# Optimization experiments

Measured on AMD Instinct MI355X. Metric: run time of the kernel, lower is better.

## Reference

```python
import jax, jax.numpy as jnp
import numpy as np
from jax import lax

DN = ('NCHW', 'OIHW', 'NCHW')
BN_EPS = 1e-5


def _conv(x, w, pad):
    # pad: list of (lo, hi) for H, W
    return lax.conv_general_dilated(x, w, (1, 1), pad, dimension_numbers=DN)


def _grid_sample_bilinear(img, grid):
    """F.grid_sample(img, grid, align_corners=True, padding_mode='zeros').
    img: [N,C,H,W], grid: [N,Ho,Wo,2] with (x,y) in [-1,1]."""
    N, C, H, W = img.shape
    gx, gy = grid[..., 0], grid[..., 1]
    # align_corners=True mapping to pixel coords
    ix = (gx + 1.0) * 0.5 * (W - 1)
    iy = (gy + 1.0) * 0.5 * (H - 1)
    x0 = jnp.floor(ix)
    y0 = jnp.floor(iy)
    x1 = x0 + 1.0
    y1 = y0 + 1.0
    # bilinear weights
    wa = (x1 - ix) * (y1 - iy)  # top-left (x0,y0)
    wb = (ix - x0) * (y1 - iy)  # top-right (x1,y0)
    wc = (x1 - ix) * (iy - y0)  # bottom-left (x0,y1)
    wd = (ix - x0) * (iy - y0)  # bottom-right (x1,y1)

    imgc = jnp.transpose(img, (0, 2, 3, 1))  # [N,H,W,C]
    b = jnp.arange(N)[:, None, None]

    def gather(xi, yi):
        valid = (xi >= 0) & (xi <= W - 1) & (yi >= 0) & (yi <= H - 1)
        xc = jnp.clip(xi, 0, W - 1).astype(jnp.int32)
        yc = jnp.clip(yi, 0, H - 1).astype(jnp.int32)
        v = imgc[b, yc, xc]  # [N,Ho,Wo,C]
        return v * valid[..., None].astype(img.dtype)

    out = (gather(x0, y0) * wa[..., None] + gather(x1, y0) * wb[..., None]
           + gather(x0, y1) * wc[..., None] + gather(x1, y1) * wd[..., None])
    return jnp.transpose(out, (0, 3, 1, 2))  # [N,C,Ho,Wo]


def setup_inputs() -> dict:
    key = jax.random.key(0)
    ks = jax.random.split(key, 12)
    N, C1, C2 = 8, 512, 256
    H, W = 64, 64
    x1 = jax.random.normal(ks[0], (N, C1, 2 * H, 2 * W), dtype=jnp.float32)
    x2 = jax.random.normal(ks[1], (N, C2, H, W), dtype=jnp.float32)
    w_change = jax.random.normal(ks[2], (C2, C1, 1, 1), dtype=jnp.float32) * 0.02
    b_change = jax.random.normal(ks[3], (C2,), dtype=jnp.float32) * 0.02
    w_cc1 = jax.random.normal(ks[4], (C2, 2 * C2, 1, 1), dtype=jnp.float32) * 0.02
    bn_gamma = 1.0 + 0.1 * jax.random.normal(ks[5], (C2,), dtype=jnp.float32)
    bn_beta = 0.1 * jax.random.normal(ks[6], (C2,), dtype=jnp.float32)
    bn_mean = 0.1 * jax.random.normal(ks[7], (C2,), dtype=jnp.float32)
    bn_var = jax.random.uniform(ks[8], (C2,), dtype=jnp.float32, minval=0.5, maxval=1.5)
    w_cc2 = jax.random.normal(ks[9], (4, C2, 3, 3), dtype=jnp.float32) * 0.02
    return {"x1": x1, "x2": x2, "w_change": w_change, "b_change": b_change,
            "w_cc1": w_cc1, "bn_gamma": bn_gamma, "bn_beta": bn_beta,
            "bn_mean": bn_mean, "bn_var": bn_var, "w_cc2": w_cc2}


def reference(x1, x2, w_change, b_change, w_cc1, bn_gamma, bn_beta, bn_mean, bn_var, w_cc2):
    # MaxPool2d(2,2)
    x1p = lax.reduce_window(x1, -jnp.inf, lax.max, (1, 1, 2, 2), (1, 1, 2, 2), 'VALID')
    # change: 1x1 conv with bias
    x1c = _conv(x1p, w_change, [(0, 0), (0, 0)]) + b_change[None, :, None, None]
    # concat + concat_conv (1x1 conv -> BN(eval) -> ReLU -> 3x3 conv)
    x = jnp.concatenate([x1c, x2], axis=1)
    x = _conv(x, w_cc1, [(0, 0), (0, 0)])
    inv = lax.rsqrt(bn_var + BN_EPS)
    x = (x - bn_mean[None, :, None, None]) * (inv * bn_gamma)[None, :, None, None] + bn_beta[None, :, None, None]
    x = jax.nn.relu(x)
    flow = _conv(x, w_cc2, [(1, 1), (1, 1)])  # [N,4,H,W]
    flow1 = flow[:, :2]
    flow2 = flow[:, 2:]

    N, _, H, W = x1c.shape
    # base grid: [...,0]=x over width, [...,1]=y over height
    xs = jnp.linspace(-1.0, 1.0, W, dtype=x1c.dtype)
    ys = jnp.linspace(-1.0, 1.0, H, dtype=x1c.dtype)
    base = jnp.stack(jnp.meshgrid(xs, ys, indexing='xy'), axis=-1)  # [H,W,2]
    norm = jnp.array([(W - 1) / 2.0, (H - 1) / 2.0], dtype=x1c.dtype)

    grid1 = base[None] + jnp.transpose(flow1, (0, 2, 3, 1)) / norm
    grid2 = base[None] + jnp.transpose(flow2, (0, 2, 3, 1)) / norm

    u1 = _grid_sample_bilinear(x1c, grid1)
    u2 = _grid_sample_bilinear(x2, grid2)
    return u1 + u2
```

## Files before the change

kernel.cpp:

```cpp
#include <hip/hip_runtime.h>
#include <hip/hip_bf16.h>

#define NB 8
#define C1 512
#define C2 256
#define HWSZ 4096
#define BN_EPS 1e-5f
#define P2 264

typedef __hip_bfloat16 bf16;
typedef __hip_bfloat162 bf162;
typedef __attribute__((ext_vector_type(8))) short short8v;
typedef __attribute__((ext_vector_type(4))) float f32x4;

static __device__ inline float b2f(bf16 h) { return __bfloat162float(h); }

static __device__ inline unsigned short f2bf(float f) {
  union { bf16 h; unsigned short u; } c;
  c.h = __float2bfloat16(f);
  return c.u;
}

static __device__ inline unsigned pack2(float a, float b) {
  union { unsigned u; bf162 h; } pk;
  pk.h = __float22bfloat162_rn(make_float2(a, b));
  return pk.u;
}

static __device__ inline uint2 pack4(float a, float b, float c, float d) {
  union { uint2 u; bf162 h[2]; } pk;
  pk.h[0] = __float22bfloat162_rn(make_float2(a, b));
  pk.h[1] = __float22bfloat162_rn(make_float2(c, d));
  return pk.u;
}

#define SBARQ() asm volatile("s_waitcnt lgkmcnt(0)\n\ts_barrier" ::: "memory")
#define SBAR()  asm volatile("s_barrier" ::: "memory")
#define LGKM0() asm volatile("s_waitcnt lgkmcnt(0)" ::: "memory")

__global__ __launch_bounds__(256) void k0_swizzle(
    const float* __restrict__ wch, const float* __restrict__ wcc1,
    unsigned short* __restrict__ wchB, unsigned short* __restrict__ wcc1B) {
  const int t = blockIdx.x * 256 + threadIdx.x;
  const int which = t >> 17;
  const int r = t & 131071;
  const int i = r & 7;
  const int lane = (r >> 3) & 63;
  const int ntile = (r >> 9) & 15;
  const int kstep = r >> 13;
  const int ci = kstep * 32 + (lane >> 4) * 8 + i;
  const int co = ntile * 16 + (lane & 15);
  const float* s = which ? wcc1 : wch;
  unsigned short* d = which ? wcc1B : wchB;
  d[r] = f2bf(s[co * 512 + ci]);
}

__global__ __launch_bounds__(512) void k12_fused(
    const float* __restrict__ x1, const float* __restrict__ x2,
    const unsigned short* __restrict__ wchB, const unsigned short* __restrict__ wcc1B,
    const float* __restrict__ bch,
    const float* __restrict__ gamma, const float* __restrict__ beta,
    const float* __restrict__ mean, const float* __restrict__ var,
    bf16* __restrict__ x1c, bf16* __restrict__ xbn) {
  __shared__ unsigned short As[64 * 40];
  __shared__ unsigned short As2[64 * P2];
  const int tid = threadIdx.x;
  const int lane = tid & 63;
  const int wv = tid >> 6;
  const int lrow = lane & 15;
  const int lgrp = lane >> 4;

  const int m0g = blockIdx.x * 64;
  const int n = m0g >> 12;
  const int hw0 = m0g & 4095;
  const int h = hw0 >> 6;

  f32x4 acc[4][2];
#pragma unroll
  for (int mt = 0; mt < 4; ++mt)
#pragma unroll
    for (int nt = 0; nt < 2; ++nt) acc[mt][nt] = (f32x4){0.f, 0.f, 0.f, 0.f};

  const int pmi = tid & 31;
  const int ms = pmi * 2;
  const int ch0 = (tid >> 5) * 2;

  const float* x1p = x1 + (size_t)n * C1 * 16384 + (size_t)(2 * h) * 128 + 2 * ms;

  float4 t0, b0, t1, b1;
#define LOADA(K0_) do { \
    const float* p_ = x1p + (size_t)((K0_) + ch0) * 16384; \
    t0 = *(const float4*)p_;            b0 = *(const float4*)(p_ + 128); \
    t1 = *(const float4*)(p_ + 16384);  b1 = *(const float4*)(p_ + 16384 + 128); \
  } while (0)
#define POOLA(U0_, U1_) do { \
    U0_ = pack2(fmaxf(fmaxf(t0.x, t0.y), fmaxf(b0.x, b0.y)), \
                fmaxf(fmaxf(t1.x, t1.y), fmaxf(b1.x, b1.y))); \
    U1_ = pack2(fmaxf(fmaxf(t0.z, t0.w), fmaxf(b0.z, b0.w)), \
                fmaxf(fmaxf(t1.z, t1.w), fmaxf(b1.z, b1.w))); \
  } while (0)

  unsigned uA0, uA1;
  LOADA(0);
  POOLA(uA0, uA1);
  LOADA(32);

  for (int ks = 0; ks < 16; ++ks) {
    SBARQ();
    *(unsigned*)&As[ms * 40 + ch0] = uA0;
    *(unsigned*)&As[(ms + 1) * 40 + ch0] = uA1;
    LGKM0();
    SBAR();

    unsigned uN0, uN1;
    if (ks < 15) {
      POOLA(uN0, uN1);
      if (ks < 14) LOADA((ks + 2) * 32);
    }

    short8v a[4];
#pragma unroll
    for (int mt = 0; mt < 4; ++mt)
      a[mt] = *(const short8v*)&As[(mt * 16 + lrow) * 40 + lgrp * 8];
#pragma unroll
    for (int nt = 0; nt < 2; ++nt) {
      const int ntile = wv * 2 + nt;
      const short8v b = *(const short8v*)&wchB[(size_t)((ks * 16 + ntile) * 64 + lane) * 8];
#pragma unroll
      for (int mt = 0; mt < 4; ++mt)
        acc[mt][nt] = __builtin_amdgcn_mfma_f32_16x16x32_bf16(a[mt], b, acc[mt][nt], 0, 0, 0);
    }
    if (ks < 15) { uA0 = uN0; uA1 = uN1; }
  }

  const int chB = tid >> 4;
  const int mqB = (tid & 15) * 4;
  float4 cf0 = *(const float4*)&x2[((size_t)(n * C2 + chB)) * HWSZ + hw0 + mqB];
  float4 cf1 = *(const float4*)&x2[((size_t)(n * C2 + 32 + chB)) * HWSZ + hw0 + mqB];

#pragma unroll
  for (int nt = 0; nt < 2; ++nt) {
    const int co = (wv * 2 + nt) * 16 + lrow;
    const float bias = bch[co];
#pragma unroll
    for (int mt = 0; mt < 4; ++mt) {
      const f32x4 v = acc[mt][nt];
      const uint2 pk = pack4(v.x + bias, v.y + bias, v.z + bias, v.w + bias);
      *(uint2*)&x1c[((size_t)(n * C2 + co)) * HWSZ + hw0 + mt * 16 + lgrp * 4] = pk;
      const int mb = mt * 16 + lgrp * 4;
      As2[(mb + 0) * P2 + co] = (unsigned short)(pk.x & 0xffffu);
      As2[(mb + 1) * P2 + co] = (unsigned short)(pk.x >> 16);
      As2[(mb + 2) * P2 + co] = (unsigned short)(pk.y & 0xffffu);
      As2[(mb + 3) * P2 + co] = (unsigned short)(pk.y >> 16);
      acc[mt][nt] = (f32x4){0.f, 0.f, 0.f, 0.f};
    }
  }
  LGKM0();
  SBAR();

#pragma unroll
  for (int ks = 0; ks < 8; ++ks) {
    short8v a[4];
#pragma unroll
    for (int mt = 0; mt < 4; ++mt)
      a[mt] = *(const short8v*)&As2[(mt * 16 + lrow) * P2 + ks * 32 + lgrp * 8];
#pragma unroll
    for (int nt = 0; nt < 2; ++nt) {
      const int ntile = wv * 2 + nt;
      const short8v b = *(const short8v*)&wcc1B[(size_t)((ks * 16 + ntile) * 64 + lane) * 8];
#pragma unroll
      for (int mt = 0; mt < 4; ++mt)
        acc[mt][nt] = __builtin_amdgcn_mfma_f32_16x16x32_bf16(a[mt], b, acc[mt][nt], 0, 0, 0);
    }
  }

  for (int ks = 8; ks < 16; ++ks) {
    const unsigned p0 = pack2(cf0.x, cf0.y);
    const unsigned p1 = pack2(cf0.z, cf0.w);
    cf0 = cf1;
    if (ks < 14) {
      cf1 = *(const float4*)&x2[((size_t)(n * C2 + (ks - 6) * 32 + chB)) * HWSZ + hw0 + mqB];
    }
    SBARQ();
    As[(mqB + 0) * 40 + chB] = (unsigned short)(p0 & 0xffffu);
    As[(mqB + 1) * 40 + chB] = (unsigned short)(p0 >> 16);
    As[(mqB + 2) * 40 + chB] = (unsigned short)(p1 & 0xffffu);
    As[(mqB + 3) * 40 + chB] = (unsigned short)(p1 >> 16);
    LGKM0();
    SBAR();

    short8v a[4];
#pragma unroll
    for (int mt = 0; mt < 4; ++mt)
      a[mt] = *(const short8v*)&As[(mt * 16 + lrow) * 40 + lgrp * 8];
#pragma unroll
    for (int nt = 0; nt < 2; ++nt) {
      const int ntile = wv * 2 + nt;
      const short8v b = *(const short8v*)&wcc1B[(size_t)((ks * 16 + ntile) * 64 + lane) * 8];
#pragma unroll
      for (int mt = 0; mt < 4; ++mt)
        acc[mt][nt] = __builtin_amdgcn_mfma_f32_16x16x32_bf16(a[mt], b, acc[mt][nt], 0, 0, 0);
    }
  }

#pragma unroll
  for (int nt = 0; nt < 2; ++nt) {
    const int co = (wv * 2 + nt) * 16 + lrow;
    const float sc = gamma[co] * rsqrtf(var[co] + BN_EPS);
    const float sh = beta[co] - mean[co] * sc;
#pragma unroll
    for (int mt = 0; mt < 4; ++mt) {
      const f32x4 vv = acc[mt][nt];
      *(uint2*)&xbn[((size_t)(n * C2 + co)) * HWSZ + hw0 + mt * 16 + lgrp * 4] =
          pack4(fmaxf(vv.x * sc + sh, 0.f), fmaxf(vv.y * sc + sh, 0.f),
                fmaxf(vv.z * sc + sh, 0.f), fmaxf(vv.w * sc + sh, 0.f));
    }
  }
#undef LOADA
#undef POOLA
}

__global__ __launch_bounds__(1024) void k34_conv_sample(
    const bf16* __restrict__ xbn, const float* __restrict__ wcc2,
    const bf16* __restrict__ x1c, const float* __restrict__ x2,
    float* __restrict__ out) {
  __shared__ float wsm[9216];
  __shared__ float part[16][4][64];
  __shared__ float flr[4][64];
  const int tid = threadIdx.x;
  const int n = blockIdx.x >> 6;
  const int h = blockIdx.x & 63;
  const int wl = tid & 63;
  const int q = tid >> 6;

  for (int idx = tid; idx < 9216; idx += 1024) {
    const int f = idx / 2304;
    const int r = idx % 2304;
    const int ci = r / 9;
    const int t = r % 9;
    wsm[ci * 36 + (t / 3) * 12 + (t % 3) * 4 + f] = wcc2[idx];
  }
  __syncthreads();

  float acc[4] = {0.f, 0.f, 0.f, 0.f};
  {
    const bf16* base = xbn + ((size_t)(n * C2 + q * 16)) * HWSZ;
    const float* wq = wsm + (q * 16) * 36;
    for (int cc = 0; cc < 16; ++cc) {
      const bf16* src = base + (size_t)cc * HWSZ;
      const float* wc = wq + cc * 36;
#pragma unroll
      for (int dy = 0; dy < 3; ++dy) {
        const int y = h + dy - 1;
        if ((unsigned)y >= 64u) continue;
        const float v = b2f(src[y * 64 + wl]);
        float vm = __shfl_up(v, 1);
        float vp = __shfl_down(v, 1);
        if (wl == 0) vm = 0.f;
        if (wl == 63) vp = 0.f;
        const float4 wa = *(const float4*)&wc[dy * 12 + 0];
        const float4 wb = *(const float4*)&wc[dy * 12 + 4];
        const float4 wd = *(const float4*)&wc[dy * 12 + 8];
        acc[0] = fmaf(vm, wa.x, fmaf(v, wb.x, fmaf(vp, wd.x, acc[0])));
        acc[1] = fmaf(vm, wa.y, fmaf(v, wb.y, fmaf(vp, wd.y, acc[1])));
        acc[2] = fmaf(vm, wa.z, fmaf(v, wb.z, fmaf(vp, wd.z, acc[2])));
        acc[3] = fmaf(vm, wa.w, fmaf(v, wb.w, fmaf(vp, wd.w, acc[3])));
      }
    }
  }
  part[q][0][wl] = acc[0];
  part[q][1][wl] = acc[1];
  part[q][2][wl] = acc[2];
  part[q][3][wl] = acc[3];
  __syncthreads();
  if (tid < 256) {
    const int f = tid >> 6;
    const int ww = tid & 63;
    float s = 0.f;
#pragma unroll
    for (int qq = 0; qq < 16; ++qq) s += part[qq][f][ww];
    flr[f][ww] = s;
  }
  __syncthreads();

  const float fx1 = flr[0][wl];
  const float fy1 = flr[1][wl];
  const float fx2 = flr[2][wl];
  const float fy2 = flr[3][wl];

  int oA1, oB1, oC1, oD1; float wa1, wb1, wc1, wd1;
  {
    const float ix = (float)wl + fx1, iy = (float)h + fy1;
    const float x0f = floorf(ix), y0f = floorf(iy);
    const float fx = ix - x0f, fy = iy - y0f;
    const int x0 = (int)x0f, y0 = (int)y0f, x1i = x0 + 1, y1i = y0 + 1;
    const float vx0 = (x0 >= 0 && x0 < 64) ? 1.f : 0.f;
    const float vx1 = (x1i >= 0 && x1i < 64) ? 1.f : 0.f;
    const float vy0 = (y0 >= 0 && y0 < 64) ? 1.f : 0.f;
    const float vy1 = (y1i >= 0 && y1i < 64) ? 1.f : 0.f;
    const int cx0 = min(max(x0, 0), 63), cx1 = min(max(x1i, 0), 63);
    const int cy0 = min(max(y0, 0), 63), cy1 = min(max(y1i, 0), 63);
    oA1 = cy0 * 64 + cx0; oB1 = cy0 * 64 + cx1;
    oC1 = cy1 * 64 + cx0; oD1 = cy1 * 64 + cx1;
    wa1 = (1.f - fx) * (1.f - fy) * vx0 * vy0;
    wb1 = fx * (1.f - fy) * vx1 * vy0;
    wc1 = (1.f - fx) * fy * vx0 * vy1;
    wd1 = fx * fy * vx1 * vy1;
  }
  int oA2, oB2, oC2, oD2; float wa2, wb2, wc2, wd2;
  {
    const float ix = (float)wl + fx2, iy = (float)h + fy2;
    const float x0f = floorf(ix), y0f = floorf(iy);
    const float fx = ix - x0f, fy = iy - y0f;
    const int x0 = (int)x0f, y0 = (int)y0f, x1i = x0 + 1, y1i = y0 + 1;
    const float vx0 = (x0 >= 0 && x0 < 64) ? 1.f : 0.f;
    const float vx1 = (x1i >= 0 && x1i < 64) ? 1.f : 0.f;
    const float vy0 = (y0 >= 0 && y0 < 64) ? 1.f : 0.f;
    const float vy1 = (y1i >= 0 && y1i < 64) ? 1.f : 0.f;
    const int cx0 = min(max(x0, 0), 63), cx1 = min(max(x1i, 0), 63);
    const int cy0 = min(max(y0, 0), 63), cy1 = min(max(y1i, 0), 63);
    oA2 = cy0 * 64 + cx0; oB2 = cy0 * 64 + cx1;
    oC2 = cy1 * 64 + cx0; oD2 = cy1 * 64 + cx1;
    wa2 = (1.f - fx) * (1.f - fy) * vx0 * vy0;
    wb2 = fx * (1.f - fy) * vx1 * vy0;
    wc2 = (1.f - fx) * fy * vx0 * vy1;
    wd2 = fx * fy * vx1 * vy1;
  }

  const bf16*  p1 = x1c + ((size_t)n * C2) * HWSZ;
  const float* p2 = x2 + ((size_t)n * C2) * HWSZ;
  const size_t obase = ((size_t)n * C2) * HWSZ + h * 64 + wl;
#pragma unroll 4
  for (int i = 0; i < 16; ++i) {
    const int co = q * 16 + i;
    const bf16*  q1 = p1 + (size_t)co * HWSZ;
    const float* q2 = p2 + (size_t)co * HWSZ;
    const float u = b2f(q1[oA1]) * wa1 + b2f(q1[oB1]) * wb1 + b2f(q1[oC1]) * wc1 + b2f(q1[oD1]) * wd1
                  + q2[oA2] * wa2 + q2[oB2] * wb2 + q2[oC2] * wc2 + q2[oD2] * wd2;
    out[obase + (size_t)co * HWSZ] = u;
  }
}

extern "C" void kernel_launch(void* const* d_in, const int* in_sizes, int n_in,
                              void* d_out, int out_size, void* d_ws, size_t ws_size,
                              hipStream_t stream) {
  const float* x1      = (const float*)d_in[0];
  const float* x2      = (const float*)d_in[1];
  const float* w_change= (const float*)d_in[2];
  const float* b_change= (const float*)d_in[3];
  const float* w_cc1   = (const float*)d_in[4];
  const float* bn_gamma= (const float*)d_in[5];
  const float* bn_beta = (const float*)d_in[6];
  const float* bn_mean = (const float*)d_in[7];
  const float* bn_var  = (const float*)d_in[8];
  const float* w_cc2   = (const float*)d_in[9];
  float* out = (float*)d_out;

  bf16*           x1c   = (bf16*)d_ws;
  bf16*           xbn   = (bf16*)((char*)d_ws + (16u << 20));
  unsigned short* wchB  = (unsigned short*)((char*)d_ws + (32u << 20));
  unsigned short* wcc1B = (unsigned short*)((char*)d_ws + (32u << 20) + (256u << 10));

  k0_swizzle<<<1024, 256, 0, stream>>>(w_change, w_cc1, wchB, wcc1B);
  k12_fused<<<512, 512, 0, stream>>>(x1, x2, wchB, wcc1B, b_change,
                                     bn_gamma, bn_beta, bn_mean, bn_var,
                                     x1c, xbn);
  k34_conv_sample<<<512, 1024, 0, stream>>>(xbn, w_cc2, x1c, x2, out);
}
```

Baseline: 141.5 us.

## Store x1c and x2 as channel-last bf16 for vectorized bilinear gathers

The fused GEMM kernel now writes x1c, and a bf16 copy of x2, in NHWC layout straight from its shared-memory tiles. The grid-sample stage can then fetch 16 contiguous channels per tap with 128-bit loads instead of doing scattered per-channel scalar gathers from NCHW planes. The costs are an extra 16 MB bf16 write of x2 and some extra stores in the producer kernel. x2 is also rounded to bf16 before sampling, which slightly changes precision.

```diff
diff --git a/kernel.cpp b/kernel.cpp
--- a/kernel.cpp
+++ b/kernel.cpp
@@ -14,6 +14,10 @@
 typedef __attribute__((ext_vector_type(4))) float f32x4;
 
 static __device__ inline float b2f(bf16 h) { return __bfloat162float(h); }
+
+static __device__ inline float us2f(unsigned short u) {
+  union { unsigned u32; float f; } c; c.u32 = ((unsigned)u) << 16; return c.f;
+}
 
 static __device__ inline unsigned short f2bf(float f) {
   union { bf16 h; unsigned short u; } c;
@@ -61,7 +65,8 @@
     const float* __restrict__ bch,
     const float* __restrict__ gamma, const float* __restrict__ beta,
     const float* __restrict__ mean, const float* __restrict__ var,
-    bf16* __restrict__ x1c, bf16* __restrict__ xbn) {
+    unsigned short* __restrict__ x1c_nhwc, unsigned short* __restrict__ x2_nhwc,
+    bf16* __restrict__ xbn) {
   __shared__ unsigned short As[64 * 40];
   __shared__ unsigned short As2[64 * P2];
   const int tid = threadIdx.x;
@@ -146,7 +151,6 @@
     for (int mt = 0; mt < 4; ++mt) {
       const f32x4 v = acc[mt][nt];
       const uint2 pk = pack4(v.x + bias, v.y + bias, v.z + bias, v.w + bias);
-      *(uint2*)&x1c[((size_t)(n * C2 + co)) * HWSZ + hw0 + mt * 16 + lgrp * 4] = pk;
       const int mb = mt * 16 + lgrp * 4;
       As2[(mb + 0) * P2 + co] = (unsigned short)(pk.x & 0xffffu);
       As2[(mb + 1) * P2 + co] = (unsigned short)(pk.x >> 16);
@@ -157,6 +161,17 @@
   }
   LGKM0();
   SBAR();
+
+  {
+    const int mm = tid >> 3;
+    const int cg = (tid & 7) * 32;
+    const size_t ob = ((size_t)(m0g + mm)) * 256 + cg;
+#pragma unroll
+    for (int k = 0; k < 4; ++k) {
+      const uint4 v = *(const uint4*)&As2[mm * P2 + cg + k * 8];
+      *(uint4*)&x1c_nhwc[ob + k * 8] = v;
+    }
+  }
 
 #pragma unroll
   for (int ks = 0; ks < 8; ++ks) {
@@ -189,6 +204,13 @@
     LGKM0();
     SBAR();
 
+    {
+      const int m = tid >> 3;
+      const int c4 = (tid & 7) * 4;
+      const uint2 v = *(const uint2*)&As[m * 40 + c4];
+      *(uint2*)&x2_nhwc[((size_t)(m0g + m)) * 256 + (ks - 8) * 32 + c4] = v;
+    }
+
     short8v a[4];
 #pragma unroll
     for (int mt = 0; mt < 4; ++mt)
@@ -222,7 +244,8 @@
 
 __global__ __launch_bounds__(1024) void k34_conv_sample(
     const bf16* __restrict__ xbn, const float* __restrict__ wcc2,
-    const bf16* __restrict__ x1c, const float* __restrict__ x2,
+    const unsigned short* __restrict__ x1c_nhwc,
+    const unsigned short* __restrict__ x2_nhwc,
     float* __restrict__ out) {
   __shared__ float wsm[9216];
   __shared__ float part[16][4][64];
@@ -327,18 +350,32 @@
     wd2 = fx * fy * vx1 * vy1;
   }
 
-  const bf16*  p1 = x1c + ((size_t)n * C2) * HWSZ;
-  const float* p2 = x2 + ((size_t)n * C2) * HWSZ;
-  const size_t obase = ((size_t)n * C2) * HWSZ + h * 64 + wl;
-#pragma unroll 4
-  for (int i = 0; i < 16; ++i) {
-    const int co = q * 16 + i;
-    const bf16*  q1 = p1 + (size_t)co * HWSZ;
-    const float* q2 = p2 + (size_t)co * HWSZ;
-    const float u = b2f(q1[oA1]) * wa1 + b2f(q1[oB1]) * wb1 + b2f(q1[oC1]) * wc1 + b2f(q1[oD1]) * wd1
-                  + q2[oA2] * wa2 + q2[oB2] * wb2 + q2[oC2] * wc2 + q2[oD2] * wd2;
-    out[obase + (size_t)co * HWSZ] = u;
-  }
+  float u[16];
+#pragma unroll
+  for (int i = 0; i < 16; ++i) u[i] = 0.f;
+
+  const unsigned short* p1 = x1c_nhwc + ((size_t)n * HWSZ) * 256 + q * 16;
+  const unsigned short* p2 = x2_nhwc + ((size_t)n * HWSZ) * 256 + q * 16;
+
+#define TAP(PB_, OFF_, WT_) do { \
+    const unsigned short* tp_ = (PB_) + (size_t)(OFF_) * 256; \
+    const uint4 v0_ = *(const uint4*)tp_; \
+    const uint4 v1_ = *(const uint4*)(tp_ + 8); \
+    const unsigned va_[8] = {v0_.x, v0_.y, v0_.z, v0_.w, v1_.x, v1_.y, v1_.z, v1_.w}; \
+    _Pragma("unroll") \
+    for (int k_ = 0; k_ < 8; ++k_) { \
+      u[2 * k_ + 0] = fmaf((WT_), us2f((unsigned short)(va_[k_] & 0xffffu)), u[2 * k_ + 0]); \
+      u[2 * k_ + 1] = fmaf((WT_), us2f((unsigned short)(va_[k_] >> 16)),    u[2 * k_ + 1]); \
+    } \
+  } while (0)
+
+  TAP(p1, oA1, wa1); TAP(p1, oB1, wb1); TAP(p1, oC1, wc1); TAP(p1, oD1, wd1);
+  TAP(p2, oA2, wa2); TAP(p2, oB2, wb2); TAP(p2, oC2, wc2); TAP(p2, oD2, wd2);
+#undef TAP
+
+  const size_t ob = ((size_t)(n * C2 + q * 16)) * HWSZ + h * 64 + wl;
+#pragma unroll
+  for (int i = 0; i < 16; ++i) out[ob + (size_t)i * HWSZ] = u[i];
 }
 
 extern "C" void kernel_launch(void* const* d_in, const int* in_sizes, int n_in,
@@ -356,14 +393,15 @@
   const float* w_cc2   = (const float*)d_in[9];
   float* out = (float*)d_out;
 
-  bf16*           x1c   = (bf16*)d_ws;
-  bf16*           xbn   = (bf16*)((char*)d_ws + (16u << 20));
-  unsigned short* wchB  = (unsigned short*)((char*)d_ws + (32u << 20));
-  unsigned short* wcc1B = (unsigned short*)((char*)d_ws + (32u << 20) + (256u << 10));
+  unsigned short* x1c_nhwc = (unsigned short*)d_ws;
+  bf16*           xbn      = (bf16*)((char*)d_ws + (16u << 20));
+  unsigned short* x2_nhwc  = (unsigned short*)((char*)d_ws + (32u << 20));
+  unsigned short* wchB     = (unsigned short*)((char*)d_ws + (48u << 20));
+  unsigned short* wcc1B    = (unsigned short*)((char*)d_ws + (48u << 20) + (256u << 10));
 
   k0_swizzle<<<1024, 256, 0, stream>>>(w_change, w_cc1, wchB, wcc1B);
   k12_fused<<<512, 512, 0, stream>>>(x1, x2, wchB, wcc1B, b_change,
                                      bn_gamma, bn_beta, bn_mean, bn_var,
-                                     x1c, xbn);
-  k34_conv_sample<<<512, 1024, 0, stream>>>(xbn, w_cc2, x1c, x2, out);
-}
+                                     x1c_nhwc, x2_nhwc, xbn);
+  k34_conv_sample<<<512, 1024, 0, stream>>>(xbn, w_cc2, x1c_nhwc, x2_nhwc, out);
+}
```

After: 142.6 us. Within noise of the previous version (+0.8%).
